# Kernel tuning notes

Hardware: AMD Instinct MI355X
Metric: run time of the kernel (lower is better)

Reference implementation:

```python
import jax, jax.numpy as jnp
import numpy as np

DEPTH = 8
DIM = 1024
DI = 2 * DIM        # d_inner (expand=2)
DSTATE = 16         # d_state
DCONV = 4           # conv kernel width
DTRANK = DIM // 16  # dt_rank = ceil(d_model/16) = 64
B = 2
L = 2048
EPS = 1e-5


def setup_inputs() -> dict:
    key = jax.random.key(0)
    ks = jax.random.split(key, 8)
    s = 0.02
    A_log = jnp.broadcast_to(
        jnp.log(jnp.arange(1, DSTATE + 1, dtype=jnp.float32)), (DEPTH, DI, DSTATE)
    )
    return {
        "x": jax.random.normal(ks[0], (B, L, DIM), jnp.float32),
        "in_proj_w": jax.random.normal(ks[1], (DEPTH, 2 * DI, DIM), jnp.float32) * s,
        "conv_w": jax.random.normal(ks[2], (DEPTH, DI, DCONV), jnp.float32) * s,
        "conv_b": jnp.zeros((DEPTH, DI), jnp.float32),
        "x_proj_w": jax.random.normal(ks[3], (DEPTH, DTRANK + 2 * DSTATE, DI), jnp.float32) * s,
        "dt_proj_w": jax.random.normal(ks[4], (DEPTH, DI, DTRANK), jnp.float32) * s,
        "dt_proj_b": jax.random.normal(ks[5], (DEPTH, DI), jnp.float32) * 0.1,
        "A_log": A_log + 0.0,
        "D": jnp.ones((DEPTH, DI), jnp.float32),
        "out_proj_w": jax.random.normal(ks[6], (DEPTH, DIM, DI), jnp.float32) * s,
        "rms_w": jnp.ones((DEPTH, DIM), jnp.float32),
    }


def _selective_scan(xs, delta, Bm, Cm, A):
    # xs, delta: [B, L, DI]; Bm, Cm: [B, L, DSTATE]; A: [DI, DSTATE]
    def step(h, t):
        dt, Bt, Ct, xt = t  # [B,DI], [B,N], [B,N], [B,DI]
        dA = jnp.exp(dt[:, :, None] * A)                      # [B,DI,N]
        h = dA * h + (dt * xt)[:, :, None] * Bt[:, None, :]   # [B,DI,N]
        y = jnp.einsum('bdn,bn->bd', h, Ct)                   # [B,DI]
        return h, y

    h0 = jnp.zeros((xs.shape[0], xs.shape[2], A.shape[1]), xs.dtype)
    ts = (delta.transpose(1, 0, 2), Bm.transpose(1, 0, 2),
          Cm.transpose(1, 0, 2), xs.transpose(1, 0, 2))
    _, ys = jax.lax.scan(step, h0, ts)  # ys: [L,B,DI]
    return ys.transpose(1, 0, 2)


def _mamba(x, Wi, cw, cb, Wx, Wdt, bdt, A_log, Dp, Wo):
    # in_proj (no bias): [B,L,DIM] -> [B,L,2*DI]
    xz = jnp.einsum('bld,ed->ble', x, Wi)
    xs, z = jnp.split(xz, 2, axis=-1)
    # depthwise causal conv1d, kernel DCONV, left pad DCONV-1
    xc = jax.lax.conv_general_dilated(
        xs.transpose(0, 2, 1), cw[:, None, :], (1,), [(DCONV - 1, 0)],
        dimension_numbers=('NCH', 'OIH', 'NCH'), feature_group_count=DI)
    xs = jax.nn.silu(xc + cb[None, :, None]).transpose(0, 2, 1)  # [B,L,DI]
    # x_proj -> dt, B, C
    xdbl = jnp.einsum('bld,ed->ble', xs, Wx)
    dt, Bm, Cm = jnp.split(xdbl, [DTRANK, DTRANK + DSTATE], axis=-1)
    delta = jax.nn.softplus(jnp.einsum('blr,dr->bld', dt, Wdt) + bdt)  # [B,L,DI]
    A = -jnp.exp(A_log)  # [DI, DSTATE]
    y = _selective_scan(xs, delta, Bm, Cm, A) + xs * Dp
    y = y * jax.nn.silu(z)
    return jnp.einsum('bld,ed->ble', y, Wo)  # out_proj, no bias


def _rmsnorm(x, w):
    return x * jax.lax.rsqrt(jnp.mean(x * x, axis=-1, keepdims=True) + EPS) * w


def reference(x, in_proj_w, conv_w, conv_b, x_proj_w, dt_proj_w, dt_proj_b,
              A_log, D, out_proj_w, rms_w):
    for i in range(DEPTH):
        x = _mamba(x, in_proj_w[i], conv_w[i], conv_b[i], x_proj_w[i],
                   dt_proj_w[i], dt_proj_b[i], A_log[i], D[i], out_proj_w[i])
        x = _rmsnorm(x, rms_w[i])
    return x
```

## Files before the change

### kernel.cpp

```cpp
#include <hip/hip_runtime.h>
#include <cstddef>

#define DEPTH  8
#define DIMM   1024
#define DI     2048
#define NST    16
#define DCONVK 4
#define DTRANK 64
#define BB     2
#define LL     2048
#define MM     (BB*LL)
#define BD     (BB*DI)
#define CHK    32
#define LC     (LL/CHK)
#define LOG2E  1.44269504088896f

typedef __attribute__((ext_vector_type(8))) short bf16x8;
typedef __attribute__((ext_vector_type(4))) float f32x4;

__device__ __forceinline__ unsigned short f2bf(float f) {
  unsigned int u = __float_as_uint(f);
  unsigned int r = (u + 0x7fffu + ((u >> 16) & 1u)) >> 16;
  return (unsigned short)r;
}
__device__ __forceinline__ float bf2f(unsigned short h) {
  return __uint_as_float(((unsigned int)h) << 16);
}

__global__ __launch_bounds__(256) void cvt2_k(const float* __restrict__ x,
                                              unsigned short* __restrict__ p,
                                              size_t n) {
  size_t i = ((size_t)blockIdx.x * 256 + threadIdx.x) * 4;
  float4 v = *(const float4*)(x + i);
  float vv[4] = {v.x, v.y, v.z, v.w};
  unsigned short u1[4], u2[4];
#pragma unroll
  for (int k = 0; k < 4; ++k) {
    unsigned short h1 = f2bf(vv[k]);
    u1[k] = h1;
    u2[k] = f2bf(vv[k] - bf2f(h1));
  }
  *(ushort4*)(p + i)     = make_ushort4(u1[0], u1[1], u1[2], u1[3]);
  *(ushort4*)(p + n + i) = make_ushort4(u2[0], u2[1], u2[2], u2[3]);
}

template <int BN, int NSPLIT>
__global__ __launch_bounds__(512, 2) void gemm3ph(
    const unsigned short* __restrict__ Ap, int lda_a, int pstr_a,
    const unsigned short* __restrict__ Bp, int lda_b, int pstr_b,
    float* __restrict__ C0, float* __restrict__ C1, int N, int Ktot) {
  constexpr int BM  = 256;
  constexpr int BF  = BN / 64;
  constexpr int BL  = BN / 128;
  constexpr int RA1 = BM * 32;
  constexpr int RB0 = 2 * BM * 32;
  constexpr int RB1 = RB0 + BN * 32;
  constexpr int BUFS = (2 * BM + 2 * BN) * 32;
  __shared__ unsigned short S[2 * BUFS];

  const int t  = threadIdx.x;
  const int w  = t >> 6;
  const int l  = t & 63;
  const int lm = l & 15;
  const int qs = ((l >> 4) << 3) ^ (((lm >> 1) & 3) << 3);

  const int nx   = gridDim.x;
  const int nwg  = nx * gridDim.y;
  const int flat = blockIdx.y * nx + blockIdx.x;
  const int swz  = (flat & 7) * (nwg >> 3) + (flat >> 3);
  const int m0 = (swz / nx) * BM;
  const int n0 = (swz % nx) * BN;
  const int z  = (NSPLIT == 2) ? blockIdx.z : 0;
  const int KS = Ktot / NSPLIT;

  const int wm = (w & 1) << 7;
  const int wn = (w >> 1) * (BN / 4);

  const int rr = t >> 2;
  const int kq = ((t & 3) ^ ((rr >> 1) & 3)) << 3;
  const unsigned short* srcA = Ap + (size_t)(m0 + rr) * lda_a + (size_t)z * KS + kq;
  const unsigned short* srcB = Bp + (size_t)(n0 + rr) * lda_b + (size_t)z * KS + kq;
  const size_t a128 = (size_t)128 * lda_a;
  const size_t b128 = (size_t)128 * lda_b;
  const int dbase = (w << 6) * 8;

#define GI(p_, off_)                                                           \
  __builtin_amdgcn_global_load_lds(                                            \
      (const __attribute__((address_space(1))) unsigned int*)(p_),             \
      (__attribute__((address_space(3))) unsigned int*)&S[bnext + (off_) + dbase], \
      16, 0, 0)

#define GI_PH0(kb_)                                                            \
  { GI(srcA + (kb_), 0); GI(srcA + a128 + (kb_), 4096);                        \
    GI(srcB + (kb_), RB0);                                                     \
    if constexpr (BL == 2) GI(srcB + b128 + (kb_), RB0 + 4096); }

#define GI_PH1(kb_)                                                            \
  { GI(srcB + (size_t)pstr_b + (kb_), RB1);                                    \
    if constexpr (BL == 2) GI(srcB + (size_t)pstr_b + b128 + (kb_), RB1 + 4096); }

#define GI_PH2(kb_)                                                            \
  { GI(srcA + (size_t)pstr_a + (kb_), RA1);                                    \
    GI(srcA + (size_t)pstr_a + a128 + (kb_), RA1 + 4096); }

  f32x4 acc[8][BF];
#pragma unroll
  for (int i = 0; i < 8; ++i)
#pragma unroll
    for (int j = 0; j < BF; ++j) acc[i][j] = (f32x4){0.f, 0.f, 0.f, 0.f};

  {
    const int bnext = 0;
    GI_PH0((size_t)0);
    GI_PH1((size_t)0);
    GI_PH2((size_t)0);
  }
  if constexpr (BN == 256) asm volatile("s_waitcnt vmcnt(4)" ::: "memory");
  else                     asm volatile("s_waitcnt vmcnt(3)" ::: "memory");
  __builtin_amdgcn_s_barrier();

  const int NT = KS >> 5;
#pragma unroll 2
  for (int ti = 0; ti < NT; ++ti) {
    const int bcur  = (ti & 1) ? BUFS : 0;
    const int bnext = (ti & 1) ? 0 : BUFS;
    const size_t kb = (size_t)((ti + 1 < NT) ? (ti + 1) : 0) * 32;
    const unsigned short* Sb = &S[bcur];
    bf16x8 a[8], b0[BF], b1[BF];

#pragma unroll
    for (int i = 0; i < 8; ++i)
      a[i] = *(const bf16x8*)&Sb[(wm + i * 16 + lm) * 32 + qs];
#pragma unroll
    for (int j = 0; j < BF; ++j)
      b0[j] = *(const bf16x8*)&Sb[RB0 + (wn + j * 16 + lm) * 32 + qs];
    GI_PH0(kb);
    if constexpr (BN == 256) asm volatile("s_waitcnt vmcnt(6)" ::: "memory");
    else                     asm volatile("s_waitcnt vmcnt(5)" ::: "memory");
    __builtin_amdgcn_s_barrier();
    asm volatile("s_waitcnt lgkmcnt(0)" ::: "memory");
    __builtin_amdgcn_s_setprio(1);
#pragma unroll
    for (int i = 0; i < 8; ++i)
#pragma unroll
      for (int j = 0; j < BF; ++j)
        acc[i][j] = __builtin_amdgcn_mfma_f32_16x16x32_bf16(a[i], b0[j], acc[i][j], 0, 0, 0);
    __builtin_amdgcn_s_setprio(0);
    __builtin_amdgcn_s_barrier();

#pragma unroll
    for (int j = 0; j < BF; ++j)
      b1[j] = *(const bf16x8*)&Sb[RB1 + (wn + j * 16 + lm) * 32 + qs];
    GI_PH1(kb);
    if constexpr (BN == 256) asm volatile("s_waitcnt vmcnt(6)" ::: "memory");
    else                     asm volatile("s_waitcnt vmcnt(4)" ::: "memory");
    __builtin_amdgcn_s_barrier();
    asm volatile("s_waitcnt lgkmcnt(0)" ::: "memory");
    __builtin_amdgcn_s_setprio(1);
#pragma unroll
    for (int i = 0; i < 8; ++i)
#pragma unroll
      for (int j = 0; j < BF; ++j)
        acc[i][j] = __builtin_amdgcn_mfma_f32_16x16x32_bf16(a[i], b1[j], acc[i][j], 0, 0, 0);
    __builtin_amdgcn_s_setprio(0);
    __builtin_amdgcn_s_barrier();

#pragma unroll
    for (int i = 0; i < 8; ++i)
      a[i] = *(const bf16x8*)&Sb[RA1 + (wm + i * 16 + lm) * 32 + qs];
    GI_PH2(kb);
    if constexpr (BN == 256) asm volatile("s_waitcnt vmcnt(4)" ::: "memory");
    else                     asm volatile("s_waitcnt vmcnt(3)" ::: "memory");
    __builtin_amdgcn_s_barrier();
    asm volatile("s_waitcnt lgkmcnt(0)" ::: "memory");
    __builtin_amdgcn_s_setprio(1);
#pragma unroll
    for (int i = 0; i < 8; ++i)
#pragma unroll
      for (int j = 0; j < BF; ++j)
        acc[i][j] = __builtin_amdgcn_mfma_f32_16x16x32_bf16(a[i], b0[j], acc[i][j], 0, 0, 0);
    __builtin_amdgcn_s_setprio(0);
    __builtin_amdgcn_s_barrier();
  }
#undef GI_PH2
#undef GI_PH1
#undef GI_PH0
#undef GI

  float* Cc = (NSPLIT == 2 && blockIdx.z) ? C1 : C0;
  const int row0 = (l >> 4) << 2;
#pragma unroll
  for (int i = 0; i < 8; ++i)
#pragma unroll
    for (int j = 0; j < BF; ++j)
#pragma unroll
      for (int r = 0; r < 4; ++r) {
        int m = m0 + wm + i * 16 + row0 + r;
        int n = n0 + wn + j * 16 + lm;
        Cc[(size_t)m * N + n] = acc[i][j][r];
      }
}

__global__ __launch_bounds__(256) void dtproj_mp(const unsigned short* __restrict__ Ap,
                                                 const unsigned short* __restrict__ Bp,
                                                 const float* __restrict__ bdt,
                                                 float* __restrict__ Cd) {
  __shared__ unsigned short S[32768];
  const int t  = threadIdx.x;
  const int w  = t >> 6;
  const int l  = t & 63;
  const int lm = l & 15;
  const int q8 = (l >> 4) << 3;
  const int qs = q8 ^ (((lm >> 1) & 3) << 3);
  const int m0 = blockIdx.y * 128;
  const int n0 = blockIdx.x * 128;
  const int wm = (w & 1) << 6;
  const int wn = (w >> 1) << 6;

#pragma unroll
  for (int it = 0; it < 16; ++it) {
    int c  = it * 256 + t;
    int kt = c >> 11;
    int c2 = c & 2047;
    const unsigned short* base;
    int r, aslot;
    if (c2 < 1024) {
      int p = c2 >> 9; int wi = c2 & 511; r = wi >> 2; aslot = wi & 3;
      base = Ap + (size_t)p * (MM * 64) + (size_t)(m0 + r) * 64;
    } else {
      int c3 = c2 - 1024;
      int p = c3 >> 9; int wi = c3 & 511; r = wi >> 2; aslot = wi & 3;
      base = Bp + (size_t)p * (DI * 64) + (size_t)(n0 + r) * 64;
    }
    int kq = (aslot ^ ((r >> 1) & 3)) << 3;
    __builtin_amdgcn_global_load_lds(
        (const __attribute__((address_space(1))) unsigned int*)(base + kt * 32 + kq),
        (__attribute__((address_space(3))) unsigned int*)&S[(size_t)(it * 256 + (w << 6)) * 8],
        16, 0, 0);
  }
  __syncthreads();

  f32x4 acc[4][4];
#pragma unroll
  for (int i = 0; i < 4; ++i)
#pragma unroll
    for (int j = 0; j < 4; ++j) acc[i][j] = (f32x4){0.f, 0.f, 0.f, 0.f};

#pragma unroll
  for (int kt = 0; kt < 2; ++kt) {
    const int RA = kt * 16384;
    const int RB = kt * 16384 + 8192;
    bf16x8 a0[4], aX[4], b0[4];
#pragma unroll
    for (int i = 0; i < 4; ++i)
      a0[i] = *(const bf16x8*)&S[RA + (wm + i * 16 + lm) * 32 + qs];
#pragma unroll
    for (int j = 0; j < 4; ++j)
      b0[j] = *(const bf16x8*)&S[RB + (wn + j * 16 + lm) * 32 + qs];
#pragma unroll
    for (int i = 0; i < 4; ++i)
#pragma unroll
      for (int j = 0; j < 4; ++j)
        acc[i][j] = __builtin_amdgcn_mfma_f32_16x16x32_bf16(a0[i], b0[j], acc[i][j], 0, 0, 0);
#pragma unroll
    for (int j = 0; j < 4; ++j)
      aX[j] = *(const bf16x8*)&S[RB + 4096 + (wn + j * 16 + lm) * 32 + qs];
#pragma unroll
    for (int i = 0; i < 4; ++i)
#pragma unroll
      for (int j = 0; j < 4; ++j)
        acc[i][j] = __builtin_amdgcn_mfma_f32_16x16x32_bf16(a0[i], aX[j], acc[i][j], 0, 0, 0);
#pragma unroll
    for (int i = 0; i < 4; ++i)
      aX[i] = *(const bf16x8*)&S[RA + 4096 + (wm + i * 16 + lm) * 32 + qs];
#pragma unroll
    for (int i = 0; i < 4; ++i)
#pragma unroll
      for (int j = 0; j < 4; ++j)
        acc[i][j] = __builtin_amdgcn_mfma_f32_16x16x32_bf16(aX[i], b0[j], acc[i][j], 0, 0, 0);
  }

  const int row0 = (l >> 4) << 2;
#pragma unroll
  for (int j = 0; j < 4; ++j) {
    int n = n0 + wn + j * 16 + lm;
    float bv = bdt[n];
#pragma unroll
    for (int i = 0; i < 4; ++i)
#pragma unroll
      for (int r = 0; r < 4; ++r) {
        int m = m0 + wm + i * 16 + row0 + r;
        float x = acc[i][j][r] + bv;
        Cd[(size_t)m * DI + n] = fmaxf(x, 0.f) + log1pf(expf(-fabsf(x)));
      }
  }
}

#define XPN 96
__global__ __launch_bounds__(256) void xproj_part_k(const float* __restrict__ A,
                                                    const float* __restrict__ W,
                                                    float* __restrict__ Cp) {
  __shared__ float As[16][128];
  __shared__ float Ws[16][XPN];
  const int t  = threadIdx.x;
  const int tx = t & 15;
  const int ty = t >> 4;
  const int m0 = blockIdx.x * 128;
  const int kb = blockIdx.y * 256;
  float acc[8][6];
#pragma unroll
  for (int i = 0; i < 8; ++i)
#pragma unroll
    for (int j = 0; j < 6; ++j) acc[i][j] = 0.f;

  for (int k0 = kb; k0 < kb + 256; k0 += 16) {
#pragma unroll
    for (int e = t; e < 512; e += 256) {
      int r = e >> 2, cq = (e & 3) << 2;
      float4 v = *(const float4*)(A + (size_t)(m0 + r) * DI + k0 + cq);
      As[cq+0][r] = v.x; As[cq+1][r] = v.y; As[cq+2][r] = v.z; As[cq+3][r] = v.w;
    }
    for (int e = t; e < 384; e += 256) {
      int r = e >> 2, cq = (e & 3) << 2;
      float4 v = *(const float4*)(W + (size_t)r * DI + k0 + cq);
      Ws[cq+0][r] = v.x; Ws[cq+1][r] = v.y; Ws[cq+2][r] = v.z; Ws[cq+3][r] = v.w;
    }
    __syncthreads();
#pragma unroll
    for (int kk = 0; kk < 16; ++kk) {
      float a[8], b[6];
#pragma unroll
      for (int i = 0; i < 8; ++i) a[i] = As[kk][ty*8 + i];
#pragma unroll
      for (int j = 0; j < 6; ++j) b[j] = Ws[kk][tx*6 + j];
#pragma unroll
      for (int i = 0; i < 8; ++i)
#pragma unroll
        for (int j = 0; j < 6; ++j) acc[i][j] += a[i] * b[j];
    }
    __syncthreads();
  }
  float* cp = Cp + (size_t)blockIdx.y * MM * XPN;
#pragma unroll
  for (int i = 0; i < 8; ++i)
#pragma unroll
    for (int j = 0; j < 6; ++j)
      cp[(size_t)(m0 + ty*8 + i) * XPN + tx*6 + j] = acc[i][j];
}

__global__ __launch_bounds__(256) void xproj_red_k(const float* __restrict__ Cp,
                                                   float* __restrict__ o,
                                                   unsigned short* __restrict__ dtp) {
  int i = blockIdx.x * 256 + threadIdx.x;
  float s = 0.f;
#pragma unroll
  for (int ks = 0; ks < 8; ++ks) s += Cp[(size_t)ks * (MM * XPN) + i];
  o[i] = s;
  int m = i / 96, col = i - m * 96;
  if (col < DTRANK) {
    unsigned short h1 = f2bf(s);
    dtp[(size_t)m * DTRANK + col] = h1;
    dtp[(size_t)MM * DTRANK + (size_t)m * DTRANK + col] = f2bf(s - bf2f(h1));
  }
}

__device__ __forceinline__ float fast_silu(float x) {
  return x * __builtin_amdgcn_rcpf(1.f + exp2f(-LOG2E * x));
}

__global__ __launch_bounds__(256) void conv_silu_k(const float* __restrict__ xz,
                                                   const float* __restrict__ cw,
                                                   const float* __restrict__ cb,
                                                   float* __restrict__ xc) {
  int idx = blockIdx.x * 256 + threadIdx.x;
  int c  = idx & (DI - 1);
  int bl = idx >> 11;
  int l  = bl & (LL - 1);
  float acc = cb[c];
#pragma unroll
  for (int k = 0; k < DCONVK; ++k) {
    int ls = l - (DCONVK - 1) + k;
    if (ls >= 0)
      acc += xz[(size_t)(bl - (DCONVK - 1) + k) * (2*DI) + c] * cw[c*DCONVK + k];
  }
  xc[idx] = fast_silu(acc);
}

__global__ __launch_bounds__(256) void scan_pass1(const float* __restrict__ delta,
                                                  const float* __restrict__ xc,
                                                  const float* __restrict__ xdbl,
                                                  const float* __restrict__ A_log,
                                                  float* __restrict__ Hc,
                                                  float* __restrict__ Sdt) {
  const int t  = threadIdx.x;
  const int g  = blockIdx.x;
  const int c  = blockIdx.y;
  const int ch = g * 256 + t;
  const int b  = ch >> 11;
  const int d  = ch & (DI - 1);
  const size_t rowbase = (size_t)b * LL + (size_t)c * LC;

  __shared__ float Bs[LC * 16];
  { int row = t >> 2, seg = t & 3;
    *(float4*)&Bs[row * 16 + seg * 4] =
        *(const float4*)(xdbl + (rowbase + row) * 96 + DTRANK + seg * 4);
  }
  __syncthreads();

  float Av[NST];
#pragma unroll
  for (int n4 = 0; n4 < 4; ++n4) {
    float4 al = *(const float4*)(A_log + (size_t)d * NST + n4 * 4);
    Av[n4*4+0] = -expf(al.x) * LOG2E;
    Av[n4*4+1] = -expf(al.y) * LOG2E;
    Av[n4*4+2] = -expf(al.z) * LOG2E;
    Av[n4*4+3] = -expf(al.w) * LOG2E;
  }
  float h[NST];
#pragma unroll
  for (int n = 0; n < NST; ++n) h[n] = 0.f;
  float S = 0.f;

#define P1_SU 4
  float aD[P1_SU], aX[P1_SU];
  float bD[P1_SU], bX[P1_SU];

#define P1_LOAD(l0, D_, X_)                                            \
  { _Pragma("unroll")                                                  \
    for (int u = 0; u < P1_SU; ++u) {                                  \
      size_t bl = rowbase + (l0) + u;                                  \
      D_[u] = delta[bl * DI + d];                                      \
      X_[u] = xc[bl * DI + d];                                         \
    } }

#define P1_COMP(l0, D_, X_)                                            \
  { _Pragma("unroll")                                                  \
    for (int u = 0; u < P1_SU; ++u) {                                  \
      float dt = D_[u], uB = dt * X_[u];                               \
      const f32x4* B4 = (const f32x4*)&Bs[((l0) + u) * 16];            \
      f32x4 B0 = B4[0], B1 = B4[1], B2 = B4[2], B3 = B4[3];            \
      _Pragma("unroll")                                                \
      for (int n = 0; n < 4; ++n) {                                    \
        h[n]      = fmaf(exp2f(dt * Av[n]),      h[n],      uB * B0[n]); \
        h[4 + n]  = fmaf(exp2f(dt * Av[4 + n]),  h[4 + n],  uB * B1[n]); \
        h[8 + n]  = fmaf(exp2f(dt * Av[8 + n]),  h[8 + n],  uB * B2[n]); \
        h[12 + n] = fmaf(exp2f(dt * Av[12 + n]), h[12 + n], uB * B3[n]); \
      }                                                                \
      S += dt;                                                         \
    } }

  P1_LOAD(0, aD, aX);
  for (int l0 = 0; l0 < LC; l0 += 2 * P1_SU) {
    P1_LOAD(l0 + P1_SU, bD, bX);
    P1_COMP(l0, aD, aX);
    if (l0 + 2 * P1_SU < LC) P1_LOAD(l0 + 2 * P1_SU, aD, aX);
    P1_COMP(l0 + P1_SU, bD, bX);
  }
#undef P1_LOAD
#undef P1_COMP

  float* hp = Hc + ((size_t)c * BD + ch) * NST;
#pragma unroll
  for (int n4 = 0; n4 < 4; ++n4)
    *(float4*)(hp + n4 * 4) =
        make_float4(h[n4*4], h[n4*4+1], h[n4*4+2], h[n4*4+3]);
  Sdt[(size_t)c * BD + ch] = S;
}

__global__ __launch_bounds__(256) void scan_pass2(float* __restrict__ Hc,
                                                  const float* __restrict__ Sdt,
                                                  const float* __restrict__ A_log) {
  const int g  = blockIdx.x * 256 + threadIdx.x;
  const int n  = g & (NST - 1);
  const int ch = g >> 4;
  const int d  = ch & (DI - 1);
  const float Av2 = -expf(A_log[d * NST + n]) * LOG2E;
  float Sv[CHK];
#pragma unroll
  for (int c = 0; c < CHK; ++c) Sv[c] = Sdt[(size_t)c * BD + ch];
  float h = 0.f;
  float tmp = Hc[(size_t)ch * NST + n];
#pragma unroll
  for (int c = 0; c < CHK; ++c) {
    size_t idx = ((size_t)c * BD + ch) * NST + n;
    float tnext = (c + 1 < CHK) ? Hc[((size_t)(c+1) * BD + ch) * NST + n] : 0.f;
    Hc[idx] = h;
    h = fmaf(exp2f(Av2 * Sv[c]), h, tmp);
    tmp = tnext;
  }
}

__global__ __launch_bounds__(256) void scan_pass3(const float* __restrict__ delta,
                                                  const float* __restrict__ xc,
                                                  const float* __restrict__ xdbl,
                                                  const float* __restrict__ A_log,
                                                  float* __restrict__ xzp,
                                                  const float* __restrict__ Dp,
                                                  const float* __restrict__ Hc) {
  const int t  = threadIdx.x;
  const int g  = blockIdx.x;
  const int c  = blockIdx.y;
  const int ch = g * 256 + t;
  const int b  = ch >> 11;
  const int d  = ch & (DI - 1);
  const size_t rowbase = (size_t)b * LL + (size_t)c * LC;

  __shared__ float BCs[LC * 32];
  {
#pragma unroll
    for (int e = t; e < 512; e += 256) {
      int row = e >> 3, seg = e & 7;
      *(float4*)&BCs[row * 32 + seg * 4] =
          *(const float4*)(xdbl + (rowbase + row) * 96 + DTRANK + seg * 4);
    }
  }
  __syncthreads();

  float Av[NST];
#pragma unroll
  for (int n4 = 0; n4 < 4; ++n4) {
    float4 al = *(const float4*)(A_log + (size_t)d * NST + n4 * 4);
    Av[n4*4+0] = -expf(al.x) * LOG2E;
    Av[n4*4+1] = -expf(al.y) * LOG2E;
    Av[n4*4+2] = -expf(al.z) * LOG2E;
    Av[n4*4+3] = -expf(al.w) * LOG2E;
  }
  const float Dv = Dp[d];
  float h[NST];
  { const float* hp = Hc + ((size_t)c * BD + ch) * NST;
#pragma unroll
    for (int n4 = 0; n4 < 4; ++n4) {
      float4 hv = *(const float4*)(hp + n4 * 4);
      h[n4*4+0] = hv.x; h[n4*4+1] = hv.y; h[n4*4+2] = hv.z; h[n4*4+3] = hv.w;
    }
  }
  unsigned short* yp = (unsigned short*)xzp;

#define P3_SU 2
  float aD[P3_SU], aX[P3_SU], aZ[P3_SU];
  float bD[P3_SU], bX[P3_SU], bZ[P3_SU];

#define P3_LOAD(l0, D_, X_, Z_)                                        \
  { _Pragma("unroll")                                                  \
    for (int u = 0; u < P3_SU; ++u) {                                  \
      size_t bl = rowbase + (l0) + u;                                  \
      D_[u] = delta[bl * DI + d];                                      \
      X_[u] = xc[bl * DI + d];                                         \
      Z_[u] = xzp[bl * (2*DI) + DI + d];                               \
    } }

#define P3_COMP(l0, D_, X_, Z_)                                        \
  { _Pragma("unroll")                                                  \
    for (int u = 0; u < P3_SU; ++u) {                                  \
      float dt = D_[u], uB = dt * X_[u];                               \
      const f32x4* R4 = (const f32x4*)&BCs[((l0) + u) * 32];           \
      f32x4 B0 = R4[0], B1 = R4[1], B2 = R4[2], B3 = R4[3];            \
      f32x4 C0 = R4[4], C1 = R4[5], C2 = R4[6], C3 = R4[7];            \
      _Pragma("unroll")                                                \
      for (int n = 0; n < 4; ++n) {                                    \
        h[n]      = fmaf(exp2f(dt * Av[n]),      h[n],      uB * B0[n]); \
        h[4 + n]  = fmaf(exp2f(dt * Av[4 + n]),  h[4 + n],  uB * B1[n]); \
        h[8 + n]  = fmaf(exp2f(dt * Av[8 + n]),  h[8 + n],  uB * B2[n]); \
        h[12 + n] = fmaf(exp2f(dt * Av[12 + n]), h[12 + n], uB * B3[n]); \
      }                                                                \
        \
      float p0 = fmaf(h[1],  C0[1], h[0]  * C0[0]);                    \
      p0 += fmaf(h[3],  C0[3], h[2]  * C0[2]);                         \
      float p1 = fmaf(h[5],  C1[1], h[4]  * C1[0]);                    \
      p1 += fmaf(h[7],  C1[3], h[6]  * C1[2]);                         \
      float p2 = fmaf(h[9],  C2[1], h[8]  * C2[0]);                    \
      p2 += fmaf(h[11], C2[3], h[10] * C2[2]);                         \
      float p3 = fmaf(h[13], C3[1], h[12] * C3[0]);                    \
      p3 += fmaf(h[15], C3[3], h[14] * C3[2]);                         \
      float s = (p0 + p1) + (p2 + p3);                                 \
      float yv = (s + X_[u] * Dv) * fast_silu(Z_[u]);                  \
      unsigned short y1 = f2bf(yv);                                    \
      size_t yb = (rowbase + (l0) + u) * 8192 + d;                     \
      yp[yb] = y1;                                                     \
      yp[yb + 2048] = f2bf(yv - bf2f(y1));                             \
    } }

  P3_LOAD(0, aD, aX, aZ);
  for (int l0 = 0; l0 < LC; l0 += 2 * P3_SU) {
    P3_LOAD(l0 + P3_SU, bD, bX, bZ);
    P3_COMP(l0, aD, aX, aZ);
    if (l0 + 2 * P3_SU < LC) P3_LOAD(l0 + 2 * P3_SU, aD, aX, aZ);
    P3_COMP(l0 + P3_SU, bD, bX, bZ);
  }
#undef P3_LOAD
#undef P3_COMP
}

template <bool PLANES>
__global__ __launch_bounds__(256) void rmsnorm_k(const float* __restrict__ x,
                                                 const float* __restrict__ x2,
                                                 const float* __restrict__ w,
                                                 float* __restrict__ o,
                                                 unsigned short* __restrict__ op) {
  int row = blockIdx.x;
  const float* xr  = x  + (size_t)row * DIMM;
  const float* x2r = x2 + (size_t)row * DIMM;
  float s = 0.f;
  for (int i = threadIdx.x; i < DIMM; i += 256) {
    float v = xr[i] + x2r[i]; s += v * v;
  }
#pragma unroll
  for (int off = 32; off > 0; off >>= 1) s += __shfl_xor(s, off, 64);
  __shared__ float red[4];
  if ((threadIdx.x & 63) == 0) red[threadIdx.x >> 6] = s;
  __syncthreads();
  float tot = red[0] + red[1] + red[2] + red[3];
  float scale = rsqrtf(tot * (1.0f / DIMM) + 1e-5f);
  for (int i = threadIdx.x; i < DIMM; i += 256) {
    float v = (xr[i] + x2r[i]) * scale * w[i];
    if (PLANES) {
      unsigned short h1 = f2bf(v);
      op[(size_t)row * DIMM + i] = h1;
      op[(size_t)MM * DIMM + (size_t)row * DIMM + i] = f2bf(v - bf2f(h1));
    } else {
      o[(size_t)row * DIMM + i] = v;
    }
  }
}

extern "C" void kernel_launch(void* const* d_in, const int* in_sizes, int n_in,
                              void* d_out, int out_size, void* d_ws, size_t ws_size,
                              hipStream_t stream) {
  (void)in_sizes; (void)n_in; (void)out_size; (void)ws_size;
  const float* x_in    = (const float*)d_in[0];
  const float* Wi_all  = (const float*)d_in[1];
  const float* cw_all  = (const float*)d_in[2];
  const float* cb_all  = (const float*)d_in[3];
  const float* Wx_all  = (const float*)d_in[4];
  const float* Wdt_all = (const float*)d_in[5];
  const float* bdt_all = (const float*)d_in[6];
  const float* Alog_all= (const float*)d_in[7];
  const float* D_all   = (const float*)d_in[8];
  const float* Wo_all  = (const float*)d_in[9];
  const float* rw_all  = (const float*)d_in[10];
  float* out = (float*)d_out;

  float* ws    = (float*)d_ws;
  float* xz    = ws;
  float* xc    = xz   + (size_t)MM * 2 * DI;
  float* xdbl  = xc   + (size_t)MM * DI;
  float* delta = xdbl + (size_t)MM * 96;
  float* xbuf  = delta+ (size_t)MM * DI;
  float* outtmp = xc;

  unsigned short* xpl  = (unsigned short*)delta;
  unsigned short* wipl = (unsigned short*)xc;
  unsigned short* wopl = (unsigned short*)(xc + (size_t)4194304);
  float*          Cp   = delta;
  float* part1 = delta + (size_t)4194304;
  float* Hc   = xbuf;
  float* Sdt  = Hc + (size_t)CHK * BD * NST;
  unsigned short* dtpl  = (unsigned short*)(xbuf + 2228224);
  unsigned short* wdtpl = (unsigned short*)(xbuf + 2490368);

  const int EW_GRID = (MM * DI) / 256;

  for (int i = 0; i < DEPTH; ++i) {
    const float* Wi   = Wi_all  + (size_t)i * (2*DI) * DIMM;
    const float* cw   = cw_all  + (size_t)i * DI * DCONVK;
    const float* cb   = cb_all  + (size_t)i * DI;
    const float* Wx   = Wx_all  + (size_t)i * 96 * DI;
    const float* Wdt  = Wdt_all + (size_t)i * DI * DTRANK;
    const float* bdt  = bdt_all + (size_t)i * DI;
    const float* Alog = Alog_all+ (size_t)i * DI * NST;
    const float* Dp   = D_all   + (size_t)i * DI;
    const float* Wo   = Wo_all  + (size_t)i * DIMM * DI;
    const float* rw   = rw_all  + (size_t)i * DIMM;

    if (i == 0)
      cvt2_k<<<(MM*DIMM)/1024, 256, 0, stream>>>(x_in, xpl, (size_t)MM * DIMM);
    cvt2_k<<<((2*DI)*DIMM)/1024, 256, 0, stream>>>(Wi, wipl, (size_t)(2*DI) * DIMM);
    gemm3ph<256,1><<<dim3((2*DI)/256, MM/256, 1), 512, 0, stream>>>(
        xpl, DIMM, MM*DIMM, wipl, DIMM, (2*DI)*DIMM, xz, nullptr, 2*DI, DIMM);
    conv_silu_k<<<EW_GRID, 256, 0, stream>>>(xz, cw, cb, xc);
    xproj_part_k<<<dim3(MM/128, 8), 256, 0, stream>>>(xc, Wx, Cp);
    xproj_red_k<<<(MM*XPN)/256, 256, 0, stream>>>(Cp, xdbl, dtpl);
    cvt2_k<<<(DI*DTRANK)/1024, 256, 0, stream>>>(Wdt, wdtpl, (size_t)DI * DTRANK);
    dtproj_mp<<<dim3(DI/128, MM/128), 256, 0, stream>>>(dtpl, wdtpl, bdt, delta);
    scan_pass1<<<dim3(BD/256, CHK), 256, 0, stream>>>(delta, xc, xdbl, Alog, Hc, Sdt);
    scan_pass2<<<(BD*NST)/256, 256, 0, stream>>>(Hc, Sdt, Alog);
    scan_pass3<<<dim3(BD/256, CHK), 256, 0, stream>>>(delta, xc, xdbl, Alog, xz, Dp, Hc);
    cvt2_k<<<(DIMM*DI)/1024, 256, 0, stream>>>(Wo, wopl, (size_t)DIMM * DI);
    gemm3ph<128,2><<<dim3(DIMM/128, MM/256, 2), 512, 0, stream>>>(
        (const unsigned short*)xz, 8192, 2048, wopl, DI, DIMM*DI,
        outtmp, part1, DIMM, DI);
    if (i < DEPTH - 1)
      rmsnorm_k<true><<<MM, 256, 0, stream>>>(outtmp, part1, rw, nullptr, xpl);
    else
      rmsnorm_k<false><<<MM, 256, 0, stream>>>(outtmp, part1, rw, out, nullptr);
  }
}
```

Before: 3.238 ms.

## Double scan chunk count, use native exp2, widen pass3 unroll

New measurement: 2.936 ms. 1.1x faster.

```diff
diff --git a/kernel.cpp b/kernel.cpp
--- a/kernel.cpp
+++ b/kernel.cpp
@@ -11,12 +11,16 @@
 #define LL     2048
 #define MM     (BB*LL)
 #define BD     (BB*DI)
-#define CHK    32
+#define CHK    64
 #define LC     (LL/CHK)
 #define LOG2E  1.44269504088896f
 
 typedef __attribute__((ext_vector_type(8))) short bf16x8;
 typedef __attribute__((ext_vector_type(4))) float f32x4;
+
+__device__ __forceinline__ float fexp2(float x) {
+  return __builtin_amdgcn_exp2f(x);
+}
 
 __device__ __forceinline__ unsigned short f2bf(float f) {
   unsigned int u = __float_as_uint(f);
@@ -365,7 +369,7 @@
 }
 
 __device__ __forceinline__ float fast_silu(float x) {
-  return x * __builtin_amdgcn_rcpf(1.f + exp2f(-LOG2E * x));
+  return x * __builtin_amdgcn_rcpf(1.f + fexp2(-LOG2E * x));
 }
 
 __global__ __launch_bounds__(256) void conv_silu_k(const float* __restrict__ xz,
@@ -401,7 +405,8 @@
   const size_t rowbase = (size_t)b * LL + (size_t)c * LC;
 
   __shared__ float Bs[LC * 16];
-  { int row = t >> 2, seg = t & 3;
+  if (t < LC * 4) {
+    int row = t >> 2, seg = t & 3;
     *(float4*)&Bs[row * 16 + seg * 4] =
         *(const float4*)(xdbl + (rowbase + row) * 96 + DTRANK + seg * 4);
   }
@@ -441,10 +446,10 @@
       f32x4 B0 = B4[0], B1 = B4[1], B2 = B4[2], B3 = B4[3];            \
       _Pragma("unroll")                                                \
       for (int n = 0; n < 4; ++n) {                                    \
-        h[n]      = fmaf(exp2f(dt * Av[n]),      h[n],      uB * B0[n]); \
-        h[4 + n]  = fmaf(exp2f(dt * Av[4 + n]),  h[4 + n],  uB * B1[n]); \
-        h[8 + n]  = fmaf(exp2f(dt * Av[8 + n]),  h[8 + n],  uB * B2[n]); \
-        h[12 + n] = fmaf(exp2f(dt * Av[12 + n]), h[12 + n], uB * B3[n]); \
+        h[n]      = fmaf(fexp2(dt * Av[n]),      h[n],      uB * B0[n]); \
+        h[4 + n]  = fmaf(fexp2(dt * Av[4 + n]),  h[4 + n],  uB * B1[n]); \
+        h[8 + n]  = fmaf(fexp2(dt * Av[8 + n]),  h[8 + n],  uB * B2[n]); \
+        h[12 + n] = fmaf(fexp2(dt * Av[12 + n]), h[12 + n], uB * B3[n]); \
       }                                                                \
       S += dt;                                                         \
     } }
@@ -485,7 +490,7 @@
     size_t idx = ((size_t)c * BD + ch) * NST + n;
     float tnext = (c + 1 < CHK) ? Hc[((size_t)(c+1) * BD + ch) * NST + n] : 0.f;
     Hc[idx] = h;
-    h = fmaf(exp2f(Av2 * Sv[c]), h, tmp);
+    h = fmaf(fexp2(Av2 * Sv[c]), h, tmp);
     tmp = tnext;
   }
 }
@@ -506,13 +511,9 @@
   const size_t rowbase = (size_t)b * LL + (size_t)c * LC;
 
   __shared__ float BCs[LC * 32];
-  {
-#pragma unroll
-    for (int e = t; e < 512; e += 256) {
-      int row = e >> 3, seg = e & 7;
-      *(float4*)&BCs[row * 32 + seg * 4] =
-          *(const float4*)(xdbl + (rowbase + row) * 96 + DTRANK + seg * 4);
-    }
+  { int row = t >> 3, seg = t & 7;
+    *(float4*)&BCs[row * 32 + seg * 4] =
+        *(const float4*)(xdbl + (rowbase + row) * 96 + DTRANK + seg * 4);
   }
   __syncthreads();
 
@@ -536,7 +537,7 @@
   }
   unsigned short* yp = (unsigned short*)xzp;
 
-#define P3_SU 2
+#define P3_SU 4
   float aD[P3_SU], aX[P3_SU], aZ[P3_SU];
   float bD[P3_SU], bX[P3_SU], bZ[P3_SU];
 
@@ -558,12 +559,12 @@
       f32x4 C0 = R4[4], C1 = R4[5], C2 = R4[6], C3 = R4[7];            \
       _Pragma("unroll")                                                \
       for (int n = 0; n < 4; ++n) {                                    \
-        h[n]      = fmaf(exp2f(dt * Av[n]),      h[n],      uB * B0[n]); \
-        h[4 + n]  = fmaf(exp2f(dt * Av[4 + n]),  h[4 + n],  uB * B1[n]); \
-        h[8 + n]  = fmaf(exp2f(dt * Av[8 + n]),  h[8 + n],  uB * B2[n]); \
-        h[12 + n] = fmaf(exp2f(dt * Av[12 + n]), h[12 + n], uB * B3[n]); \
+        h[n]      = fmaf(fexp2(dt * Av[n]),      h[n],      uB * B0[n]); \
+        h[4 + n]  = fmaf(fexp2(dt * Av[4 + n]),  h[4 + n],  uB * B1[n]); \
+        h[8 + n]  = fmaf(fexp2(dt * Av[8 + n]),  h[8 + n],  uB * B2[n]); \
+        h[12 + n] = fmaf(fexp2(dt * Av[12 + n]), h[12 + n], uB * B3[n]); \
       }                                                                \
-        \
+                  \
       float p0 = fmaf(h[1],  C0[1], h[0]  * C0[0]);                    \
       p0 += fmaf(h[3],  C0[3], h[2]  * C0[2]);                         \
       float p1 = fmaf(h[5],  C1[1], h[4]  * C1[0]);                    \
@@ -654,9 +655,9 @@
   float*          Cp   = delta;
   float* part1 = delta + (size_t)4194304;
   float* Hc   = xbuf;
-  float* Sdt  = Hc + (size_t)CHK * BD * NST;
-  unsigned short* dtpl  = (unsigned short*)(xbuf + 2228224);
-  unsigned short* wdtpl = (unsigned short*)(xbuf + 2490368);
+  unsigned short* dtpl  = (unsigned short*)out;
+  unsigned short* wdtpl = (unsigned short*)(out + 262144);
+  float* Sdt  = out + 393216;
 
   const int EW_GRID = (MM * DI) / 256;
 
```
